# Kernel optimization log

Measured on AMD Instinct MI355X. Metric: run time of the kernel, lower is better.

## Reference

```python
import jax, jax.numpy as jnp
import numpy as np

NB = 256  # images are quantized to 256 intensity levels (uint8 pipeline)


def _histograms(q):
    # q: int32 (BC, N) values in [0, NB)
    BC, N = q.shape
    idx = (q + jnp.arange(BC, dtype=jnp.int32)[:, None] * NB).reshape(-1)
    ones = jnp.ones((BC * N,), dtype=jnp.int32)
    return jax.ops.segment_sum(ones, idx, num_segments=BC * NB).reshape(BC, NB)


def _match_lut(counts_s, counts_r):
    # Fixed-shape emulation of the per-channel np.unique/cumsum/np.interp loop.
    occ_s = counts_s > 0
    occ_r = counts_r > 0
    first_s = jnp.argmax(occ_s)  # smallest unique source value (dropped, maps to 0)
    first_r = jnp.argmax(occ_r)  # smallest unique reference value (dropped)
    cs = counts_s.at[first_s].set(0)
    cr = counts_r.at[first_r].set(0)
    cums = jnp.cumsum(cs).astype(jnp.float32)
    cumr = jnp.cumsum(cr).astype(jnp.float32)
    s_q = cums / jnp.maximum(cums[-1], 1.0)  # source quantiles at every bin
    r_q = cumr / jnp.maximum(cumr[-1], 1.0)
    # Compact occupied reference bins (excluding the first) to the front so that
    # jnp.interp sees only the quantiles/values that np.unique would produce.
    occ_r2 = occ_r & (jnp.arange(NB) != first_r)
    order = jnp.argsort(jnp.logical_not(occ_r2))  # stable: occupied bins first, ascending
    occ_sorted = occ_r2[order]
    xp = jnp.where(occ_sorted, r_q[order], 2.0)   # pad with x>1 so queries (<=1) never reach pads
    fp = jnp.where(occ_sorted, order.astype(jnp.float32), 0.0)
    lut = jnp.trunc(jnp.interp(s_q, xp, fp))  # trunc == C-style cast into uint8 result buffer
    lut = lut.at[first_s].set(0.0)            # interp_value[0] = 0 in the original
    ok = (jnp.sum(occ_s) > 1) & (jnp.sum(occ_r) > 1)  # 'continue' branch -> zeros
    return jnp.where(ok, lut, 0.0)


def _match_histogram(source, reference):
    # source/reference: float (B,3,H,W) with values at exact 0..255 levels
    B, C, H, W = source.shape
    sq = jnp.clip(jnp.round(source), 0, NB - 1).astype(jnp.int32).reshape(B * C, H * W)
    rq = jnp.clip(jnp.round(reference), 0, NB - 1).astype(jnp.int32).reshape(B * C, H * W)
    lut = jax.vmap(_match_lut)(_histograms(sq), _histograms(rq))  # (BC, NB)
    return jnp.take_along_axis(lut, sq, axis=1).reshape(B, C, H, W)


def reference(input_data, target_data, ref_data, mask_src, mask_tar):
    to_img = lambda x: (x + 1.0) * 0.5 * 255.0  # tensor2image(x) * 255
    inp = to_img(input_data)
    tar = to_img(target_data)
    ref = to_img(ref_data)
    m_src = jnp.broadcast_to(mask_src, inp.shape)
    m_tar = jnp.broadcast_to(mask_tar, tar.shape)
    input_masked = inp * m_src
    target_masked = tar * m_tar
    ref_masked = ref * m_src
    matched = jax.lax.stop_gradient(_match_histogram(ref_masked, target_masked))
    input_match = matched * m_src
    return jnp.mean(jnp.abs(input_masked - input_match))  # L1Loss


def setup_inputs() -> dict:
    key = jax.random.key(0)
    k1, k2, k3, k4, k5 = jax.random.split(key, 5)
    B, H, W = 8, 512, 512

    def img(k):
        # exact multiples of 1/255 in [-1,1] -> integer 0..255 after tensor2image*255
        levels = jax.random.randint(k, (B, 3, H, W), 0, 256).astype(jnp.float32)
        return (levels / 255.0) * 2.0 - 1.0

    def mask(k):
        return (jax.random.uniform(k, (B, 1, H, W)) > 0.3).astype(jnp.float32)

    return {
        "input_data": img(k1),
        "target_data": img(k2),
        "ref_data": img(k3),
        "mask_src": mask(k4),
        "mask_tar": mask(k5),
    }
```

## Files before the change

kernel.cpp:

```cpp
#include <hip/hip_runtime.h>
#include <hip/hip_bf16.h>

#define HW    262144
#define HW4   65536
#define BC    24
#define NB    256
#define NTOT  6291456

#define GH    64
#define GL    64

#define WS_HSP_OFF  0
#define WS_HRP_OFF  1572864
#define WS_LSUM_OFF 3145728
#define WS_LUT_OFF  3151872

__device__ __forceinline__ int quantize(float x, float m) {
    float v = (x + 1.0f) * 0.5f * 255.0f * m;
    float r = rintf(v);
    r = fminf(fmaxf(r, 0.0f), 255.0f);
    return (int)r;
}

__device__ __forceinline__ int incl_scan256(int v, int t, int* buf) {
    buf[t] = v;
    __syncthreads();
#pragma unroll
    for (int off = 1; off < NB; off <<= 1) {
        int x = (t >= off) ? buf[t - off] : 0;
        __syncthreads();
        buf[t] += x;
        __syncthreads();
    }
    return buf[t];
}

__global__ void __launch_bounds__(256)
hist_kernel(const float4* __restrict__ ref4,
            const float4* __restrict__ tar4,
            const float4* __restrict__ ms4,
            const float4* __restrict__ mt4,
            int* __restrict__ hsPart, int* __restrict__ hrPart) {
    __shared__ int wh[4 * 2 * NB];
    const int t = threadIdx.x;
    const int wave = t >> 6;
    const int lane = t & 63;
#pragma unroll
    for (int j = 0; j < 8; ++j) wh[t + j * 256] = 0;
    __syncthreads();

    const int c = blockIdx.y;
    const int b = c / 3;
    const float4* refc = ref4 + (size_t)c * HW4;
    const float4* tarc = tar4 + (size_t)c * HW4;
    const float4* msb  = ms4 + (size_t)b * HW4;
    const float4* mtb  = mt4 + (size_t)b * HW4;

    const int base = blockIdx.x * 256 + t;

    float4 R[4], T[4], M[4], MT[4];
#pragma unroll
    for (int j = 0; j < 4; ++j) R[j]  = refc[base + j * 16384];
#pragma unroll
    for (int j = 0; j < 4; ++j) M[j]  = msb[base + j * 16384];
#pragma unroll
    for (int j = 0; j < 4; ++j) T[j]  = tarc[base + j * 16384];
#pragma unroll
    for (int j = 0; j < 4; ++j) MT[j] = mtb[base + j * 16384];

    int* whS = &wh[wave * 512];
    int* whR = &wh[wave * 512 + 256];
    int n0s = 0, n0r = 0;
#pragma unroll
    for (int j = 0; j < 4; ++j) {
        const float rv[4]  = {R[j].x, R[j].y, R[j].z, R[j].w};
        const float mv[4]  = {M[j].x, M[j].y, M[j].z, M[j].w};
        const float tvv[4] = {T[j].x, T[j].y, T[j].z, T[j].w};
        const float mtv[4] = {MT[j].x, MT[j].y, MT[j].z, MT[j].w};
#pragma unroll
        for (int k = 0; k < 4; ++k) {
            if (mv[k] != 0.0f) atomicAdd(&whS[quantize(rv[k], mv[k])], 1);
            else n0s++;
            if (mtv[k] != 0.0f) atomicAdd(&whR[quantize(tvv[k], mtv[k])], 1);
            else n0r++;
        }
    }
#pragma unroll
    for (int off = 32; off > 0; off >>= 1) {
        n0s += __shfl_down(n0s, off);
        n0r += __shfl_down(n0r, off);
    }
    if (lane == 0) {
        if (n0s) atomicAdd(&whS[0], n0s);
        if (n0r) atomicAdd(&whR[0], n0r);
    }
    __syncthreads();

    const int s = wh[t] + wh[512 + t] + wh[1024 + t] + wh[1536 + t];
    const int r = wh[256 + t] + wh[768 + t] + wh[1280 + t] + wh[1792 + t];
    hsPart[(c * GH + blockIdx.x) * NB + t] = s;
    hrPart[(c * GH + blockIdx.x) * NB + t] = r;
}

__global__ void __launch_bounds__(256)
lut_kernel(const int* __restrict__ hsPart,
           const int* __restrict__ hrPart,
           float* __restrict__ lut) {
    const int c = blockIdx.x;
    const int t = threadIdx.x;

    __shared__ int buf[NB];
    __shared__ float xp[NB];
    __shared__ float fp[NB];
    __shared__ int firstS, firstR, nOccS, nOccR;

    int cs = 0, cr = 0;
#pragma unroll 4
    for (int g = 0; g < GH; ++g) {
        cs += hsPart[(c * GH + g) * NB + t];
        cr += hrPart[(c * GH + g) * NB + t];
    }

    if (t == 0) { firstS = NB; firstR = NB; nOccS = 0; nOccR = 0; }
    __syncthreads();
    if (cs > 0) { atomicMin(&firstS, t); atomicAdd(&nOccS, 1); }
    if (cr > 0) { atomicMin(&firstR, t); atomicAdd(&nOccR, 1); }
    __syncthreads();

    const int csz = (t == firstS) ? 0 : cs;
    const int crz = (t == firstR) ? 0 : cr;

    const int cumS = incl_scan256(csz, t, buf);
    const int totS = buf[NB - 1];
    __syncthreads();
    const int cumR = incl_scan256(crz, t, buf);
    const int totR = buf[NB - 1];
    __syncthreads();
    const int occ2 = (cr > 0 && t != firstR) ? 1 : 0;
    const int rank = incl_scan256(occ2, t, buf) - occ2;
    __syncthreads();

    const float x  = (float)cumS / fmaxf((float)totS, 1.0f);
    const float rq = (float)cumR / fmaxf((float)totR, 1.0f);

    xp[t] = 2.0f;
    fp[t] = 0.0f;
    __syncthreads();
    if (occ2) { xp[rank] = rq; fp[rank] = (float)t; }
    __syncthreads();

    int lo = 0, hi = NB;
    while (lo < hi) {
        int mid = (lo + hi) >> 1;
        if (xp[mid] > x) hi = mid; else lo = mid + 1;
    }
    int i = lo;
    i = (i < 1) ? 1 : ((i > NB - 1) ? NB - 1 : i);
    float dxv = xp[i] - xp[i - 1];
    float f;
    if (dxv == 0.0f) f = fp[i];
    else f = fp[i - 1] + (x - xp[i - 1]) / dxv * (fp[i] - fp[i - 1]);
    if (x < xp[0]) f = fp[0];

    float l = truncf(f);
    if (t == firstS) l = 0.0f;
    if (!((nOccS > 1) && (nOccR > 1))) l = 0.0f;

    lut[c * NB + t] = l;
}

__global__ void __launch_bounds__(256)
loss_kernel(const float4* __restrict__ inp4,
            const float4* __restrict__ ref4,
            const float4* __restrict__ ms4,
            const float* __restrict__ lut,
            float* __restrict__ lsum) {
    __shared__ float llut[NB];
    const int t = threadIdx.x;
    const int c = blockIdx.y;
    const int b = c / 3;
    llut[t] = lut[c * NB + t];
    __syncthreads();

    const float4* inpc = inp4 + (size_t)c * HW4;
    const float4* refc = ref4 + (size_t)c * HW4;
    const float4* msb  = ms4 + (size_t)b * HW4;

    const int base = blockIdx.x * 256 + t;

    float4 X[4], R[4], M[4];
#pragma unroll
    for (int j = 0; j < 4; ++j) X[j] = inpc[base + j * 16384];
#pragma unroll
    for (int j = 0; j < 4; ++j) R[j] = refc[base + j * 16384];
#pragma unroll
    for (int j = 0; j < 4; ++j) M[j] = msb[base + j * 16384];

    float s = 0.0f;
#pragma unroll
    for (int j = 0; j < 4; ++j) {
        const float xv[4] = {X[j].x, X[j].y, X[j].z, X[j].w};
        const float rv[4] = {R[j].x, R[j].y, R[j].z, R[j].w};
        const float mv[4] = {M[j].x, M[j].y, M[j].z, M[j].w};
#pragma unroll
        for (int k = 0; k < 4; ++k) {
            const int q = quantize(rv[k], mv[k]);
            const float im = (xv[k] + 1.0f) * 127.5f;
            s += mv[k] * fabsf(im - llut[q]);
        }
    }

#pragma unroll
    for (int off = 32; off > 0; off >>= 1) s += __shfl_down(s, off);
    __shared__ float wsum[4];
    const int lane = t & 63;
    const int wave = t >> 6;
    if (lane == 0) wsum[wave] = s;
    __syncthreads();
    if (t == 0)
        lsum[c * GL + blockIdx.x] = wsum[0] + wsum[1] + wsum[2] + wsum[3];
}

__global__ void __launch_bounds__(256)
finalize_kernel(const float* __restrict__ lsum, float* __restrict__ out) {
    const int t = threadIdx.x;
    float s = 0.0f;
#pragma unroll
    for (int i = t; i < BC * GL; i += 256) s += lsum[i];
#pragma unroll
    for (int off = 32; off > 0; off >>= 1) s += __shfl_down(s, off);
    __shared__ float wsum[4];
    const int lane = t & 63;
    const int wave = t >> 6;
    if (lane == 0) wsum[wave] = s;
    __syncthreads();
    if (t == 0)
        out[0] = (wsum[0] + wsum[1] + wsum[2] + wsum[3]) / (float)NTOT;
}

extern "C" void kernel_launch(void* const* d_in, const int* in_sizes, int n_in,
                              void* d_out, int out_size, void* d_ws, size_t ws_size,
                              hipStream_t stream) {
    const float* inp  = (const float*)d_in[0];
    const float* tar  = (const float*)d_in[1];
    const float* ref  = (const float*)d_in[2];
    const float* msrc = (const float*)d_in[3];
    const float* mtar = (const float*)d_in[4];

    char* ws = (char*)d_ws;
    int*   hsPart = (int*)(ws + WS_HSP_OFF);
    int*   hrPart = (int*)(ws + WS_HRP_OFF);
    float* lsum   = (float*)(ws + WS_LSUM_OFF);
    float* lut    = (float*)(ws + WS_LUT_OFF);

    hist_kernel<<<dim3(GH, BC), 256, 0, stream>>>(
        (const float4*)ref, (const float4*)tar,
        (const float4*)msrc, (const float4*)mtar, hsPart, hrPart);

    lut_kernel<<<BC, 256, 0, stream>>>(hsPart, hrPart, lut);

    loss_kernel<<<dim3(GL, BC), 256, 0, stream>>>(
        (const float4*)inp, (const float4*)ref, (const float4*)msrc,
        lut, lsum);

    finalize_kernel<<<1, 256, 0, stream>>>(lsum, (float*)d_out);
}
```

Baseline: 132.8 us.

## Fuse histogram, LUT, loss and reduction into one cooperative persistent kernel

Replaces four kernel launches with a single cooperative kernel of 1008 blocks that uses grid-wide syncs between the histogram, LUT construction, loss and final reduction phases. Each thread keeps its quantized reference values and mask bits packed in registers from the histogram pass, so the loss pass only needs to reload the input tensor and not ref or mask. This is meant to remove launch gaps and roughly a third of the global traffic in the second pass. In exchange it adds three grid barriers, leaves most blocks idle during the LUT phase, and depends on all blocks being co-resident.

```diff
diff --git a/kernel.cpp b/kernel.cpp
--- a/kernel.cpp
+++ b/kernel.cpp
@@ -1,19 +1,23 @@
 #include <hip/hip_runtime.h>
-#include <hip/hip_bf16.h>
-
-#define HW    262144
-#define HW4   65536
-#define BC    24
-#define NB    256
-#define NTOT  6291456
-
-#define GH    64
-#define GL    64
+#include <hip/hip_cooperative_groups.h>
+
+namespace cg = cooperative_groups;
+
+#define HW     262144
+#define HW4    65536
+#define BC     24
+#define NB     256
+#define NTOT   6291456
+
+#define GPC    42
+#define NBLK   (BC * GPC)
+#define STRIDE (GPC * 256)
+#define NIT    7
 
 #define WS_HSP_OFF  0
-#define WS_HRP_OFF  1572864
-#define WS_LSUM_OFF 3145728
-#define WS_LUT_OFF  3151872
+#define WS_HRP_OFF  (NBLK * NB * 4)
+#define WS_LUT_OFF  (2 * NBLK * NB * 4)
+#define WS_LSUM_OFF (2 * NBLK * NB * 4 + BC * NB * 4)
 
 __device__ __forceinline__ int quantize(float x, float m) {
     float v = (x + 1.0f) * 0.5f * 255.0f * m;
@@ -35,54 +39,75 @@
     return buf[t];
 }
 
-__global__ void __launch_bounds__(256)
-hist_kernel(const float4* __restrict__ ref4,
-            const float4* __restrict__ tar4,
-            const float4* __restrict__ ms4,
-            const float4* __restrict__ mt4,
-            int* __restrict__ hsPart, int* __restrict__ hrPart) {
-    __shared__ int wh[4 * 2 * NB];
-    const int t = threadIdx.x;
+__global__ void __launch_bounds__(256, 4)
+fused_kernel(const float4* __restrict__ inp4,
+             const float4* __restrict__ tar4,
+             const float4* __restrict__ ref4,
+             const float4* __restrict__ ms4,
+             const float4* __restrict__ mt4,
+             int* __restrict__ hsPart, int* __restrict__ hrPart,
+             float* __restrict__ lut, float* __restrict__ lsum,
+             float* __restrict__ out) {
+    cg::grid_group grid = cg::this_grid();
+
+    __shared__ int   wh[4 * 2 * NB];
+    __shared__ int   buf[NB];
+    __shared__ float xp[NB];
+    __shared__ float fp[NB];
+    __shared__ float llut[NB];
+    __shared__ float wsum[4];
+    __shared__ int firstS, firstR, nOccS, nOccR;
+
+    const int t    = threadIdx.x;
     const int wave = t >> 6;
     const int lane = t & 63;
+    const int cb   = blockIdx.x;
+    const int c    = cb / GPC;
+    const int g    = cb % GPC;
+    const int b    = c / 3;
+
 #pragma unroll
     for (int j = 0; j < 8; ++j) wh[t + j * 256] = 0;
     __syncthreads();
 
-    const int c = blockIdx.y;
-    const int b = c / 3;
     const float4* refc = ref4 + (size_t)c * HW4;
     const float4* tarc = tar4 + (size_t)c * HW4;
     const float4* msb  = ms4 + (size_t)b * HW4;
     const float4* mtb  = mt4 + (size_t)b * HW4;
 
-    const int base = blockIdx.x * 256 + t;
-
-    float4 R[4], T[4], M[4], MT[4];
-#pragma unroll
-    for (int j = 0; j < 4; ++j) R[j]  = refc[base + j * 16384];
-#pragma unroll
-    for (int j = 0; j < 4; ++j) M[j]  = msb[base + j * 16384];
-#pragma unroll
-    for (int j = 0; j < 4; ++j) T[j]  = tarc[base + j * 16384];
-#pragma unroll
-    for (int j = 0; j < 4; ++j) MT[j] = mtb[base + j * 16384];
-
     int* whS = &wh[wave * 512];
     int* whR = &wh[wave * 512 + 256];
+
+    const int base0 = g * 256 + t;
+
+    unsigned qp[NIT];
+    unsigned mbv = 0;
     int n0s = 0, n0r = 0;
-#pragma unroll
-    for (int j = 0; j < 4; ++j) {
-        const float rv[4]  = {R[j].x, R[j].y, R[j].z, R[j].w};
-        const float mv[4]  = {M[j].x, M[j].y, M[j].z, M[j].w};
-        const float tvv[4] = {T[j].x, T[j].y, T[j].z, T[j].w};
-        const float mtv[4] = {MT[j].x, MT[j].y, MT[j].z, MT[j].w};
-#pragma unroll
-        for (int k = 0; k < 4; ++k) {
-            if (mv[k] != 0.0f) atomicAdd(&whS[quantize(rv[k], mv[k])], 1);
-            else n0s++;
-            if (mtv[k] != 0.0f) atomicAdd(&whR[quantize(tvv[k], mtv[k])], 1);
-            else n0r++;
+
+#pragma unroll
+    for (int j = 0; j < NIT; ++j) {
+        const int i = base0 + j * STRIDE;
+        qp[j] = 0u;
+        if (i < HW4) {
+            const float4 R  = refc[i];
+            const float4 M  = msb[i];
+            const float4 T  = tarc[i];
+            const float4 MT = mtb[i];
+            const float rv[4]  = {R.x, R.y, R.z, R.w};
+            const float mv[4]  = {M.x, M.y, M.z, M.w};
+            const float tv[4]  = {T.x, T.y, T.z, T.w};
+            const float mtv[4] = {MT.x, MT.y, MT.z, MT.w};
+            unsigned q4 = 0;
+#pragma unroll
+            for (int k = 0; k < 4; ++k) {
+                const int qs = quantize(rv[k], mv[k]);
+                q4 |= ((unsigned)qs) << (8 * k);
+                if (mv[k] != 0.0f) { atomicAdd(&whS[qs], 1); mbv |= 1u << (4 * j + k); }
+                else n0s++;
+                if (mtv[k] != 0.0f) atomicAdd(&whR[quantize(tv[k], mtv[k])], 1);
+                else n0r++;
+            }
+            qp[j] = q4;
         }
     }
 #pragma unroll
@@ -96,172 +121,128 @@
     }
     __syncthreads();
 
-    const int s = wh[t] + wh[512 + t] + wh[1024 + t] + wh[1536 + t];
-    const int r = wh[256 + t] + wh[768 + t] + wh[1280 + t] + wh[1792 + t];
-    hsPart[(c * GH + blockIdx.x) * NB + t] = s;
-    hrPart[(c * GH + blockIdx.x) * NB + t] = r;
-}
-
-__global__ void __launch_bounds__(256)
-lut_kernel(const int* __restrict__ hsPart,
-           const int* __restrict__ hrPart,
-           float* __restrict__ lut) {
-    const int c = blockIdx.x;
-    const int t = threadIdx.x;
-
-    __shared__ int buf[NB];
-    __shared__ float xp[NB];
-    __shared__ float fp[NB];
-    __shared__ int firstS, firstR, nOccS, nOccR;
-
-    int cs = 0, cr = 0;
-#pragma unroll 4
-    for (int g = 0; g < GH; ++g) {
-        cs += hsPart[(c * GH + g) * NB + t];
-        cr += hrPart[(c * GH + g) * NB + t];
-    }
-
-    if (t == 0) { firstS = NB; firstR = NB; nOccS = 0; nOccR = 0; }
-    __syncthreads();
-    if (cs > 0) { atomicMin(&firstS, t); atomicAdd(&nOccS, 1); }
-    if (cr > 0) { atomicMin(&firstR, t); atomicAdd(&nOccR, 1); }
-    __syncthreads();
-
-    const int csz = (t == firstS) ? 0 : cs;
-    const int crz = (t == firstR) ? 0 : cr;
-
-    const int cumS = incl_scan256(csz, t, buf);
-    const int totS = buf[NB - 1];
-    __syncthreads();
-    const int cumR = incl_scan256(crz, t, buf);
-    const int totR = buf[NB - 1];
-    __syncthreads();
-    const int occ2 = (cr > 0 && t != firstR) ? 1 : 0;
-    const int rank = incl_scan256(occ2, t, buf) - occ2;
-    __syncthreads();
-
-    const float x  = (float)cumS / fmaxf((float)totS, 1.0f);
-    const float rq = (float)cumR / fmaxf((float)totR, 1.0f);
-
-    xp[t] = 2.0f;
-    fp[t] = 0.0f;
-    __syncthreads();
-    if (occ2) { xp[rank] = rq; fp[rank] = (float)t; }
-    __syncthreads();
-
-    int lo = 0, hi = NB;
-    while (lo < hi) {
-        int mid = (lo + hi) >> 1;
-        if (xp[mid] > x) hi = mid; else lo = mid + 1;
-    }
-    int i = lo;
-    i = (i < 1) ? 1 : ((i > NB - 1) ? NB - 1 : i);
-    float dxv = xp[i] - xp[i - 1];
-    float f;
-    if (dxv == 0.0f) f = fp[i];
-    else f = fp[i - 1] + (x - xp[i - 1]) / dxv * (fp[i] - fp[i - 1]);
-    if (x < xp[0]) f = fp[0];
-
-    float l = truncf(f);
-    if (t == firstS) l = 0.0f;
-    if (!((nOccS > 1) && (nOccR > 1))) l = 0.0f;
-
-    lut[c * NB + t] = l;
-}
-
-__global__ void __launch_bounds__(256)
-loss_kernel(const float4* __restrict__ inp4,
-            const float4* __restrict__ ref4,
-            const float4* __restrict__ ms4,
-            const float* __restrict__ lut,
-            float* __restrict__ lsum) {
-    __shared__ float llut[NB];
-    const int t = threadIdx.x;
-    const int c = blockIdx.y;
-    const int b = c / 3;
+    const int hs = wh[t] + wh[512 + t] + wh[1024 + t] + wh[1536 + t];
+    const int hr = wh[256 + t] + wh[768 + t] + wh[1280 + t] + wh[1792 + t];
+    hsPart[cb * NB + t] = hs;
+    hrPart[cb * NB + t] = hr;
+
+    grid.sync();
+
+    if (cb < BC) {
+        int cs = 0, cr = 0;
+#pragma unroll 6
+        for (int gg = 0; gg < GPC; ++gg) {
+            cs += hsPart[(cb * GPC + gg) * NB + t];
+            cr += hrPart[(cb * GPC + gg) * NB + t];
+        }
+
+        if (t == 0) { firstS = NB; firstR = NB; nOccS = 0; nOccR = 0; }
+        __syncthreads();
+        if (cs > 0) { atomicMin(&firstS, t); atomicAdd(&nOccS, 1); }
+        if (cr > 0) { atomicMin(&firstR, t); atomicAdd(&nOccR, 1); }
+        __syncthreads();
+
+        const int csz = (t == firstS) ? 0 : cs;
+        const int crz = (t == firstR) ? 0 : cr;
+
+        const int cumS = incl_scan256(csz, t, buf);
+        const int totS = buf[NB - 1];
+        __syncthreads();
+        const int cumR = incl_scan256(crz, t, buf);
+        const int totR = buf[NB - 1];
+        __syncthreads();
+        const int occ2 = (cr > 0 && t != firstR) ? 1 : 0;
+        const int rank = incl_scan256(occ2, t, buf) - occ2;
+        __syncthreads();
+
+        const float x  = (float)cumS / fmaxf((float)totS, 1.0f);
+        const float rq = (float)cumR / fmaxf((float)totR, 1.0f);
+
+        xp[t] = 2.0f;
+        fp[t] = 0.0f;
+        __syncthreads();
+        if (occ2) { xp[rank] = rq; fp[rank] = (float)t; }
+        __syncthreads();
+
+        int lo = 0, hi = NB;
+        while (lo < hi) {
+            int mid = (lo + hi) >> 1;
+            if (xp[mid] > x) hi = mid; else lo = mid + 1;
+        }
+        int i2 = lo;
+        i2 = (i2 < 1) ? 1 : ((i2 > NB - 1) ? NB - 1 : i2);
+        float dxv = xp[i2] - xp[i2 - 1];
+        float f;
+        if (dxv == 0.0f) f = fp[i2];
+        else f = fp[i2 - 1] + (x - xp[i2 - 1]) / dxv * (fp[i2] - fp[i2 - 1]);
+        if (x < xp[0]) f = fp[0];
+
+        float l = truncf(f);
+        if (t == firstS) l = 0.0f;
+        if (!((nOccS > 1) && (nOccR > 1))) l = 0.0f;
+
+        lut[cb * NB + t] = l;
+    }
+
+    grid.sync();
+
     llut[t] = lut[c * NB + t];
     __syncthreads();
 
     const float4* inpc = inp4 + (size_t)c * HW4;
-    const float4* refc = ref4 + (size_t)c * HW4;
-    const float4* msb  = ms4 + (size_t)b * HW4;
-
-    const int base = blockIdx.x * 256 + t;
-
-    float4 X[4], R[4], M[4];
-#pragma unroll
-    for (int j = 0; j < 4; ++j) X[j] = inpc[base + j * 16384];
-#pragma unroll
-    for (int j = 0; j < 4; ++j) R[j] = refc[base + j * 16384];
-#pragma unroll
-    for (int j = 0; j < 4; ++j) M[j] = msb[base + j * 16384];
-
     float s = 0.0f;
 #pragma unroll
-    for (int j = 0; j < 4; ++j) {
-        const float xv[4] = {X[j].x, X[j].y, X[j].z, X[j].w};
-        const float rv[4] = {R[j].x, R[j].y, R[j].z, R[j].w};
-        const float mv[4] = {M[j].x, M[j].y, M[j].z, M[j].w};
-#pragma unroll
-        for (int k = 0; k < 4; ++k) {
-            const int q = quantize(rv[k], mv[k]);
-            const float im = (xv[k] + 1.0f) * 127.5f;
-            s += mv[k] * fabsf(im - llut[q]);
-        }
-    }
-
+    for (int j = 0; j < NIT; ++j) {
+        const int i = base0 + j * STRIDE;
+        if (i < HW4) {
+            const float4 X = inpc[i];
+            const float xv[4] = {X.x, X.y, X.z, X.w};
+#pragma unroll
+            for (int k = 0; k < 4; ++k) {
+                const int q = (qp[j] >> (8 * k)) & 255;
+                const float mf = (float)((mbv >> (4 * j + k)) & 1u);
+                const float im = (xv[k] + 1.0f) * 127.5f;
+                s += mf * fabsf(im - llut[q]);
+            }
+        }
+    }
 #pragma unroll
     for (int off = 32; off > 0; off >>= 1) s += __shfl_down(s, off);
-    __shared__ float wsum[4];
-    const int lane = t & 63;
-    const int wave = t >> 6;
     if (lane == 0) wsum[wave] = s;
     __syncthreads();
-    if (t == 0)
-        lsum[c * GL + blockIdx.x] = wsum[0] + wsum[1] + wsum[2] + wsum[3];
-}
-
-__global__ void __launch_bounds__(256)
-finalize_kernel(const float* __restrict__ lsum, float* __restrict__ out) {
-    const int t = threadIdx.x;
-    float s = 0.0f;
-#pragma unroll
-    for (int i = t; i < BC * GL; i += 256) s += lsum[i];
-#pragma unroll
-    for (int off = 32; off > 0; off >>= 1) s += __shfl_down(s, off);
-    __shared__ float wsum[4];
-    const int lane = t & 63;
-    const int wave = t >> 6;
-    if (lane == 0) wsum[wave] = s;
-    __syncthreads();
-    if (t == 0)
-        out[0] = (wsum[0] + wsum[1] + wsum[2] + wsum[3]) / (float)NTOT;
+    if (t == 0) lsum[cb] = wsum[0] + wsum[1] + wsum[2] + wsum[3];
+
+    grid.sync();
+
+    if (cb == 0) {
+        float ss = 0.0f;
+        for (int i = t; i < NBLK; i += 256) ss += lsum[i];
+#pragma unroll
+        for (int off = 32; off > 0; off >>= 1) ss += __shfl_down(ss, off);
+        if (lane == 0) wsum[wave] = ss;
+        __syncthreads();
+        if (t == 0) out[0] = (wsum[0] + wsum[1] + wsum[2] + wsum[3]) / (float)NTOT;
+    }
 }
 
 extern "C" void kernel_launch(void* const* d_in, const int* in_sizes, int n_in,
                               void* d_out, int out_size, void* d_ws, size_t ws_size,
                               hipStream_t stream) {
-    const float* inp  = (const float*)d_in[0];
-    const float* tar  = (const float*)d_in[1];
-    const float* ref  = (const float*)d_in[2];
-    const float* msrc = (const float*)d_in[3];
-    const float* mtar = (const float*)d_in[4];
+    const float4* inp = (const float4*)d_in[0];
+    const float4* tar = (const float4*)d_in[1];
+    const float4* ref = (const float4*)d_in[2];
+    const float4* ms  = (const float4*)d_in[3];
+    const float4* mt  = (const float4*)d_in[4];
 
     char* ws = (char*)d_ws;
     int*   hsPart = (int*)(ws + WS_HSP_OFF);
     int*   hrPart = (int*)(ws + WS_HRP_OFF);
+    float* lut    = (float*)(ws + WS_LUT_OFF);
     float* lsum   = (float*)(ws + WS_LSUM_OFF);
-    float* lut    = (float*)(ws + WS_LUT_OFF);
-
-    hist_kernel<<<dim3(GH, BC), 256, 0, stream>>>(
-        (const float4*)ref, (const float4*)tar,
-        (const float4*)msrc, (const float4*)mtar, hsPart, hrPart);
-
-    lut_kernel<<<BC, 256, 0, stream>>>(hsPart, hrPart, lut);
-
-    loss_kernel<<<dim3(GL, BC), 256, 0, stream>>>(
-        (const float4*)inp, (const float4*)ref, (const float4*)msrc,
-        lut, lsum);
-
-    finalize_kernel<<<1, 256, 0, stream>>>(lsum, (float*)d_out);
-}
+    float* outp   = (float*)d_out;
+
+    void* args[] = {&inp, &tar, &ref, &ms, &mt,
+                    &hsPart, &hrPart, &lut, &lsum, &outp};
+    hipLaunchCooperativeKernel(reinterpret_cast<void*>(fused_kernel),
+                               dim3(NBLK), dim3(256), args, 0, stream);
+}
```

Result: slower. 443.8 us (+234.3%).

## Cache packed quantized values and fuse LUT build and finalize into loss kernel

Applied to the files above, without the earlier changes.

The histogram kernel now writes a packed 16-bit quantized value plus mask bit per pixel, so the loss kernel reads 2 bytes instead of re-reading the reference image and mask floats. LUT construction is folded into every loss block, with each block redundantly reducing the 64 partial histograms for its channel. The final reduction runs in the last-arriving block through an atomic counter, which removes two kernel launches. In exchange every loss block repeats the LUT work, and the packed buffer costs an extra write.

```diff
diff --git a/kernel.cpp b/kernel.cpp
--- a/kernel.cpp
+++ b/kernel.cpp
@@ -1,5 +1,4 @@
 #include <hip/hip_runtime.h>
-#include <hip/hip_bf16.h>
 
 #define HW    262144
 #define HW4   65536
@@ -9,11 +8,13 @@
 
 #define GH    64
 #define GL    64
+#define TOTL  (BC * GL)
 
 #define WS_HSP_OFF  0
 #define WS_HRP_OFF  1572864
-#define WS_LSUM_OFF 3145728
-#define WS_LUT_OFF  3151872
+#define WS_QM_OFF   3145728
+#define WS_LSUM_OFF 15728640
+#define WS_CNT_OFF  15734784
 
 __device__ __forceinline__ int quantize(float x, float m) {
     float v = (x + 1.0f) * 0.5f * 255.0f * m;
@@ -40,11 +41,15 @@
             const float4* __restrict__ tar4,
             const float4* __restrict__ ms4,
             const float4* __restrict__ mt4,
-            int* __restrict__ hsPart, int* __restrict__ hrPart) {
+            int* __restrict__ hsPart, int* __restrict__ hrPart,
+            ushort4* __restrict__ qm, unsigned* __restrict__ counter) {
     __shared__ int wh[4 * 2 * NB];
     const int t = threadIdx.x;
     const int wave = t >> 6;
     const int lane = t & 63;
+
+    if (blockIdx.x == 0 && blockIdx.y == 0 && t == 0) *counter = 0u;
+
 #pragma unroll
     for (int j = 0; j < 8; ++j) wh[t + j * 256] = 0;
     __syncthreads();
@@ -55,6 +60,7 @@
     const float4* tarc = tar4 + (size_t)c * HW4;
     const float4* msb  = ms4 + (size_t)b * HW4;
     const float4* mtb  = mt4 + (size_t)b * HW4;
+    ushort4* qmc = qm + (size_t)c * HW4;
 
     const int base = blockIdx.x * 256 + t;
 
@@ -77,13 +83,23 @@
         const float mv[4]  = {M[j].x, M[j].y, M[j].z, M[j].w};
         const float tvv[4] = {T[j].x, T[j].y, T[j].z, T[j].w};
         const float mtv[4] = {MT[j].x, MT[j].y, MT[j].z, MT[j].w};
+        unsigned u16[4];
 #pragma unroll
         for (int k = 0; k < 4; ++k) {
-            if (mv[k] != 0.0f) atomicAdd(&whS[quantize(rv[k], mv[k])], 1);
+            const int qs = quantize(rv[k], mv[k]);
+            const bool ms_on = (mv[k] != 0.0f);
+            u16[k] = (unsigned)qs | (ms_on ? 256u : 0u);
+            if (ms_on) atomicAdd(&whS[qs], 1);
             else n0s++;
             if (mtv[k] != 0.0f) atomicAdd(&whR[quantize(tvv[k], mtv[k])], 1);
             else n0r++;
         }
+        ushort4 qq;
+        qq.x = (unsigned short)u16[0];
+        qq.y = (unsigned short)u16[1];
+        qq.z = (unsigned short)u16[2];
+        qq.w = (unsigned short)u16[3];
+        qmc[base + j * 16384] = qq;
     }
 #pragma unroll
     for (int off = 32; off > 0; off >>= 1) {
@@ -103,22 +119,41 @@
 }
 
 __global__ void __launch_bounds__(256)
-lut_kernel(const int* __restrict__ hsPart,
-           const int* __restrict__ hrPart,
-           float* __restrict__ lut) {
-    const int c = blockIdx.x;
-    const int t = threadIdx.x;
-
-    __shared__ int buf[NB];
+loss_kernel(const float4* __restrict__ inp4,
+            const int* __restrict__ hsPart,
+            const int* __restrict__ hrPart,
+            const ushort4* __restrict__ qm,
+            float* __restrict__ lsum,
+            unsigned* __restrict__ counter,
+            float* __restrict__ out) {
+    __shared__ int   buf[NB];
     __shared__ float xp[NB];
     __shared__ float fp[NB];
-    __shared__ int firstS, firstR, nOccS, nOccR;
+    __shared__ float llut[NB];
+    __shared__ float wsum[4];
+    __shared__ int firstS, firstR, nOccS, nOccR, isLast;
+
+    const int t = threadIdx.x;
+    const int c = blockIdx.y;
+    const int g = blockIdx.x;
+    const int lane = t & 63;
+    const int wave = t >> 6;
+
+    const float4*  inpc = inp4 + (size_t)c * HW4;
+    const ushort4* qmc  = qm + (size_t)c * HW4;
+    const int base = g * 256 + t;
+    float4  X[4];
+    ushort4 Q[4];
+#pragma unroll
+    for (int j = 0; j < 4; ++j) X[j] = inpc[base + j * 16384];
+#pragma unroll
+    for (int j = 0; j < 4; ++j) Q[j] = qmc[base + j * 16384];
 
     int cs = 0, cr = 0;
 #pragma unroll 4
-    for (int g = 0; g < GH; ++g) {
-        cs += hsPart[(c * GH + g) * NB + t];
-        cr += hrPart[(c * GH + g) * NB + t];
+    for (int gg = 0; gg < GH; ++gg) {
+        cs += hsPart[(c * GH + gg) * NB + t];
+        cr += hrPart[(c * GH + gg) * NB + t];
     }
 
     if (t == 0) { firstS = NB; firstR = NB; nOccS = 0; nOccR = 0; }
@@ -154,88 +189,59 @@
         int mid = (lo + hi) >> 1;
         if (xp[mid] > x) hi = mid; else lo = mid + 1;
     }
-    int i = lo;
-    i = (i < 1) ? 1 : ((i > NB - 1) ? NB - 1 : i);
-    float dxv = xp[i] - xp[i - 1];
+    int i2 = lo;
+    i2 = (i2 < 1) ? 1 : ((i2 > NB - 1) ? NB - 1 : i2);
+    float dxv = xp[i2] - xp[i2 - 1];
     float f;
-    if (dxv == 0.0f) f = fp[i];
-    else f = fp[i - 1] + (x - xp[i - 1]) / dxv * (fp[i] - fp[i - 1]);
+    if (dxv == 0.0f) f = fp[i2];
+    else f = fp[i2 - 1] + (x - xp[i2 - 1]) / dxv * (fp[i2] - fp[i2 - 1]);
     if (x < xp[0]) f = fp[0];
 
     float l = truncf(f);
     if (t == firstS) l = 0.0f;
     if (!((nOccS > 1) && (nOccR > 1))) l = 0.0f;
 
-    lut[c * NB + t] = l;
-}
-
-__global__ void __launch_bounds__(256)
-loss_kernel(const float4* __restrict__ inp4,
-            const float4* __restrict__ ref4,
-            const float4* __restrict__ ms4,
-            const float* __restrict__ lut,
-            float* __restrict__ lsum) {
-    __shared__ float llut[NB];
-    const int t = threadIdx.x;
-    const int c = blockIdx.y;
-    const int b = c / 3;
-    llut[t] = lut[c * NB + t];
-    __syncthreads();
-
-    const float4* inpc = inp4 + (size_t)c * HW4;
-    const float4* refc = ref4 + (size_t)c * HW4;
-    const float4* msb  = ms4 + (size_t)b * HW4;
-
-    const int base = blockIdx.x * 256 + t;
-
-    float4 X[4], R[4], M[4];
-#pragma unroll
-    for (int j = 0; j < 4; ++j) X[j] = inpc[base + j * 16384];
-#pragma unroll
-    for (int j = 0; j < 4; ++j) R[j] = refc[base + j * 16384];
-#pragma unroll
-    for (int j = 0; j < 4; ++j) M[j] = msb[base + j * 16384];
+    llut[t] = l;
+    __syncthreads();
 
     float s = 0.0f;
 #pragma unroll
     for (int j = 0; j < 4; ++j) {
         const float xv[4] = {X[j].x, X[j].y, X[j].z, X[j].w};
-        const float rv[4] = {R[j].x, R[j].y, R[j].z, R[j].w};
-        const float mv[4] = {M[j].x, M[j].y, M[j].z, M[j].w};
+        const unsigned qv[4] = {Q[j].x, Q[j].y, Q[j].z, Q[j].w};
 #pragma unroll
         for (int k = 0; k < 4; ++k) {
-            const int q = quantize(rv[k], mv[k]);
+            const int q = (int)(qv[k] & 255u);
+            const float mf = (float)((qv[k] >> 8) & 1u);
             const float im = (xv[k] + 1.0f) * 127.5f;
-            s += mv[k] * fabsf(im - llut[q]);
+            s += mf * fabsf(im - llut[q]);
         }
     }
 
 #pragma unroll
     for (int off = 32; off > 0; off >>= 1) s += __shfl_down(s, off);
-    __shared__ float wsum[4];
-    const int lane = t & 63;
-    const int wave = t >> 6;
     if (lane == 0) wsum[wave] = s;
     __syncthreads();
-    if (t == 0)
-        lsum[c * GL + blockIdx.x] = wsum[0] + wsum[1] + wsum[2] + wsum[3];
-}
-
-__global__ void __launch_bounds__(256)
-finalize_kernel(const float* __restrict__ lsum, float* __restrict__ out) {
-    const int t = threadIdx.x;
-    float s = 0.0f;
-#pragma unroll
-    for (int i = t; i < BC * GL; i += 256) s += lsum[i];
-#pragma unroll
-    for (int off = 32; off > 0; off >>= 1) s += __shfl_down(s, off);
-    __shared__ float wsum[4];
-    const int lane = t & 63;
-    const int wave = t >> 6;
-    if (lane == 0) wsum[wave] = s;
-    __syncthreads();
-    if (t == 0)
-        out[0] = (wsum[0] + wsum[1] + wsum[2] + wsum[3]) / (float)NTOT;
+    if (t == 0) {
+        lsum[c * GL + g] = wsum[0] + wsum[1] + wsum[2] + wsum[3];
+        __threadfence();
+        unsigned old = atomicAdd(counter, 1u);
+        isLast = (old == (unsigned)(TOTL - 1)) ? 1 : 0;
+    }
+    __syncthreads();
+
+    if (isLast) {
+        float ss = 0.0f;
+#pragma unroll 2
+        for (int i = t; i < TOTL; i += 256)
+            ss += atomicAdd(&lsum[i], 0.0f);
+#pragma unroll
+        for (int off = 32; off > 0; off >>= 1) ss += __shfl_down(ss, off);
+        if (lane == 0) wsum[wave] = ss;
+        __syncthreads();
+        if (t == 0)
+            out[0] = (wsum[0] + wsum[1] + wsum[2] + wsum[3]) / (float)NTOT;
+    }
 }
 
 extern "C" void kernel_launch(void* const* d_in, const int* in_sizes, int n_in,
@@ -248,20 +254,17 @@
     const float* mtar = (const float*)d_in[4];
 
     char* ws = (char*)d_ws;
-    int*   hsPart = (int*)(ws + WS_HSP_OFF);
-    int*   hrPart = (int*)(ws + WS_HRP_OFF);
-    float* lsum   = (float*)(ws + WS_LSUM_OFF);
-    float* lut    = (float*)(ws + WS_LUT_OFF);
+    int*      hsPart  = (int*)(ws + WS_HSP_OFF);
+    int*      hrPart  = (int*)(ws + WS_HRP_OFF);
+    ushort4*  qm      = (ushort4*)(ws + WS_QM_OFF);
+    float*    lsum    = (float*)(ws + WS_LSUM_OFF);
+    unsigned* counter = (unsigned*)(ws + WS_CNT_OFF);
 
     hist_kernel<<<dim3(GH, BC), 256, 0, stream>>>(
         (const float4*)ref, (const float4*)tar,
-        (const float4*)msrc, (const float4*)mtar, hsPart, hrPart);
-
-    lut_kernel<<<BC, 256, 0, stream>>>(hsPart, hrPart, lut);
+        (const float4*)msrc, (const float4*)mtar,
+        hsPart, hrPart, qm, counter);
 
     loss_kernel<<<dim3(GL, BC), 256, 0, stream>>>(
-        (const float4*)inp, (const float4*)ref, (const float4*)msrc,
-        lut, lsum);
-
-    finalize_kernel<<<1, 256, 0, stream>>>(lsum, (float*)d_out);
-}
+        (const float4*)inp, hsPart, hrPart, qm, lsum, counter, (float*)d_out);
+}
```

Result: slower. 174.4 us (+31.4%).
